# Kernel optimization log

Hardware: AMD Instinct MI355X
Metric: run time of the kernel (lower is better)

Reference implementation:

```python
import jax, jax.numpy as jnp
import numpy as np

B = 32768
F = 256
H1 = 16
H2 = 8

def setup_inputs() -> dict:
    key = jax.random.key(0)
    ks = jax.random.split(key, 9)
    x = jax.random.normal(ks[0], (B, F), dtype=jnp.float32)
    # Stacked per-feature MLP params (one UnivariateNetwork per feature)
    W1 = jax.random.normal(ks[1], (F, H1), dtype=jnp.float32) * (1.0 / np.sqrt(1))
    b1 = jax.random.normal(ks[2], (F, H1), dtype=jnp.float32) * 0.05
    W2 = jax.random.normal(ks[3], (F, H1, H2), dtype=jnp.float32) * (1.0 / np.sqrt(H1))
    b2 = jax.random.normal(ks[4], (F, H2), dtype=jnp.float32) * 0.05
    W3 = jax.random.normal(ks[5], (F, H2), dtype=jnp.float32) * (1.0 / np.sqrt(H2))
    b3 = jax.random.normal(ks[6], (F,), dtype=jnp.float32) * 0.05
    theta = jax.random.uniform(ks[7], (F,), dtype=jnp.float32) * 0.05
    bias = jnp.zeros((1,), dtype=jnp.float32)
    return {"x": x, "W1": W1, "b1": b1, "W2": W2, "b2": b2,
            "W3": W3, "b3": b3, "theta": theta, "bias": bias}

def reference(x, W1, b1, W2, b2, W3, b3, theta, bias):
    # Batched per-feature MLP: 1 -> H1 -> H2 -> 1 with ELU, all features at once.
    h1 = jax.nn.elu(x[:, :, None] * W1[None, :, :] + b1[None, :, :])      # [B, F, H1]
    h2 = jax.nn.elu(jnp.einsum('bfh,fhk->bfk', h1, W2) + b2[None, :, :])  # [B, F, H2]
    Z = jnp.einsum('bfk,fk->bf', h2, W3) + b3[None, :]                    # [B, F]
    weights = jax.nn.softplus(theta)                                      # [F]
    y_pred = Z @ weights + bias                                           # [B]
    return (y_pred, weights, Z)
```

## Files before the change

### kernel.cpp

```cpp
#include <hip/hip_runtime.h>

#define NB 32768
#define NF 256
#define H1 16
#define H2 8
#define R_PER_BLOCK 64
#define CHUNK 16

__device__ __forceinline__ float elu_f(float v) {
    return v > 0.0f ? v : (__expf(v) - 1.0f);
}

__attribute__((amdgpu_waves_per_eu(2, 2)))
__global__ __launch_bounds__(256)
void nul_kernel(const float* __restrict__ x,
                const float* __restrict__ W1, const float* __restrict__ b1,
                const float* __restrict__ W2, const float* __restrict__ b2,
                const float* __restrict__ W3, const float* __restrict__ b3,
                const float* __restrict__ theta, const float* __restrict__ bias,
                float* __restrict__ y_out, float* __restrict__ w_out,
                float* __restrict__ z_out) {
    const int f = threadIdx.x;
    const int rowBase = blockIdx.x * R_PER_BLOCK;

    float w1v[H1], b1v[H1], w2v[H1 * H2], b2v[H2], w3v[H2];
    {
        const float4* p = reinterpret_cast<const float4*>(W1 + f * H1);
        #pragma unroll
        for (int i = 0; i < H1 / 4; ++i) {
            float4 v = p[i];
            w1v[4*i] = v.x; w1v[4*i+1] = v.y; w1v[4*i+2] = v.z; w1v[4*i+3] = v.w;
        }
    }
    {
        const float4* p = reinterpret_cast<const float4*>(b1 + f * H1);
        #pragma unroll
        for (int i = 0; i < H1 / 4; ++i) {
            float4 v = p[i];
            b1v[4*i] = v.x; b1v[4*i+1] = v.y; b1v[4*i+2] = v.z; b1v[4*i+3] = v.w;
        }
    }
    {
        const float4* p = reinterpret_cast<const float4*>(W2 + f * H1 * H2);
        #pragma unroll
        for (int i = 0; i < (H1 * H2) / 4; ++i) {
            float4 v = p[i];
            w2v[4*i] = v.x; w2v[4*i+1] = v.y; w2v[4*i+2] = v.z; w2v[4*i+3] = v.w;
        }
    }
    {
        const float4* p = reinterpret_cast<const float4*>(b2 + f * H2);
        #pragma unroll
        for (int i = 0; i < H2 / 4; ++i) {
            float4 v = p[i];
            b2v[4*i] = v.x; b2v[4*i+1] = v.y; b2v[4*i+2] = v.z; b2v[4*i+3] = v.w;
        }
    }
    {
        const float4* p = reinterpret_cast<const float4*>(W3 + f * H2);
        #pragma unroll
        for (int i = 0; i < H2 / 4; ++i) {
            float4 v = p[i];
            w3v[4*i] = v.x; w3v[4*i+1] = v.y; w3v[4*i+2] = v.z; w3v[4*i+3] = v.w;
        }
    }
    const float b3v   = b3[f];
    const float th    = theta[f];
    const float wv    = __logf(1.0f + __expf(th));
    const float biasv = bias[0];

    if (blockIdx.x == 0) w_out[f] = wv;

    __shared__ float P[CHUNK][NF + 1];

    float xnext = x[rowBase * NF + f];

    for (int c = 0; c < R_PER_BLOCK; c += CHUNK) {
        #pragma unroll 1
        for (int r = 0; r < CHUNK; ++r) {
            const int row = rowBase + c + r;
            const float xv = xnext;
            int nrow = row + 1; if (nrow >= NB) nrow = row;
            xnext = x[nrow * NF + f];

            float h1v[H1];
            #pragma unroll
            for (int h = 0; h < H1; ++h)
                h1v[h] = elu_f(fmaf(xv, w1v[h], b1v[h]));

            float acc[H2];
            #pragma unroll
            for (int k = 0; k < H2; ++k) acc[k] = b2v[k];
            #pragma unroll
            for (int h = 0; h < H1; ++h) {
                #pragma unroll
                for (int k = 0; k < H2; ++k)
                    acc[k] = fmaf(h1v[h], w2v[h * H2 + k], acc[k]);
            }

            float z = b3v;
            #pragma unroll
            for (int k = 0; k < H2; ++k)
                z = fmaf(elu_f(acc[k]), w3v[k], z);

            z_out[row * NF + f] = z;
            P[r][f] = wv * z;
        }
        __syncthreads();
        {
            const int rr = threadIdx.x >> 4;
            const int l  = threadIdx.x & 15;
            float s = 0.0f;
            #pragma unroll
            for (int i = 0; i < 16; ++i) s += P[rr][i * 16 + l];
            #pragma unroll
            for (int o = 8; o > 0; o >>= 1) s += __shfl_down(s, o, 16);
            if (l == 0) y_out[rowBase + c + rr] = s + biasv;
        }
        __syncthreads();
    }
}

extern "C" void kernel_launch(void* const* d_in, const int* in_sizes, int n_in,
                              void* d_out, int out_size, void* d_ws, size_t ws_size,
                              hipStream_t stream) {
    const float* x     = (const float*)d_in[0];
    const float* W1    = (const float*)d_in[1];
    const float* b1    = (const float*)d_in[2];
    const float* W2    = (const float*)d_in[3];
    const float* b2    = (const float*)d_in[4];
    const float* W3    = (const float*)d_in[5];
    const float* b3    = (const float*)d_in[6];
    const float* theta = (const float*)d_in[7];
    const float* bias  = (const float*)d_in[8];

    float* y_out = (float*)d_out;
    float* w_out = y_out + NB;
    float* z_out = w_out + NF;

    nul_kernel<<<NB / R_PER_BLOCK, NF, 0, stream>>>(
        x, W1, b1, W2, b2, W3, b3, theta, bias, y_out, w_out, z_out);
}
```

Before: 149.6 us.

## Tile by feature groups with shared-memory weights and atomic row reduction

Replaces the one-thread-per-feature kernel, which kept all weights in registers, with a 2D grid. Each block handles 16 features and 128 rows, stages the weights in LDS, and has each thread process 8 rows in an unrolled loop to get more independent work per thread. The y reduction now uses 16-lane shuffles plus float atomics into y_out, which a separate init kernel fills with the bias first and which also computes the softplus weights. In exchange the change adds a second launch, atomic traffic, a non-deterministic summation order, and reads of x and writes of z that touch only 64 bytes per row.

```diff
diff --git a/kernel.cpp b/kernel.cpp
--- a/kernel.cpp
+++ b/kernel.cpp
@@ -4,120 +4,132 @@
 #define NF 256
 #define H1 16
 #define H2 8
-#define R_PER_BLOCK 64
-#define CHUNK 16
+#define FG 16
+#define RJ 8
+#define ROWS_PER_BLOCK (16 * RJ)
 
 __device__ __forceinline__ float elu_f(float v) {
     return v > 0.0f ? v : (__expf(v) - 1.0f);
 }
 
-__attribute__((amdgpu_waves_per_eu(2, 2)))
 __global__ __launch_bounds__(256)
-void nul_kernel(const float* __restrict__ x,
-                const float* __restrict__ W1, const float* __restrict__ b1,
-                const float* __restrict__ W2, const float* __restrict__ b2,
-                const float* __restrict__ W3, const float* __restrict__ b3,
-                const float* __restrict__ theta, const float* __restrict__ bias,
-                float* __restrict__ y_out, float* __restrict__ w_out,
-                float* __restrict__ z_out) {
-    const int f = threadIdx.x;
-    const int rowBase = blockIdx.x * R_PER_BLOCK;
+void nul_init(const float* __restrict__ theta, const float* __restrict__ bias,
+              float* __restrict__ y_out, float* __restrict__ w_out) {
+    const int t = blockIdx.x * 256 + threadIdx.x;
+    if (t < NB) y_out[t] = bias[0];
+    if (t < NF) w_out[t] = __logf(1.0f + __expf(theta[t]));
+}
 
-    float w1v[H1], b1v[H1], w2v[H1 * H2], b2v[H2], w3v[H2];
+__global__ __launch_bounds__(256)
+void nul_main(const float* __restrict__ x,
+              const float* __restrict__ W1, const float* __restrict__ b1,
+              const float* __restrict__ W2, const float* __restrict__ b2,
+              const float* __restrict__ W3, const float* __restrict__ b3,
+              const float* __restrict__ theta,
+              float* __restrict__ y_out, float* __restrict__ z_out) {
+    __shared__ __align__(16) float sW1[FG][17];
+    __shared__ __align__(16) float sB1[FG][17];
+    __shared__ __align__(16) float sW2[FG][132];
+    __shared__ __align__(16) float sB2[FG][12];
+    __shared__ __align__(16) float sW3[FG][12];
+    __shared__ float sB3[FG];
+    __shared__ float sWv[FG];
+
+    const int tid  = threadIdx.x;
+    const int f0   = blockIdx.y * FG;
+    const int row0 = blockIdx.x * ROWS_PER_BLOCK;
+
     {
-        const float4* p = reinterpret_cast<const float4*>(W1 + f * H1);
+        const int f = tid >> 4, h = tid & 15;
+        sW1[f][h] = W1[(f0 + f) * H1 + h];
+        sB1[f][h] = b1[(f0 + f) * H1 + h];
+    }
+    {
+        const int e = tid * 8;
+        const int ff = e >> 7, c = e & 127;
+        const float4* p = reinterpret_cast<const float4*>(W2 + (f0 + ff) * (H1 * H2) + c);
+        float4 v0 = p[0], v1 = p[1];
+        float* d = &sW2[ff][c];
+        d[0] = v0.x; d[1] = v0.y; d[2] = v0.z; d[3] = v0.w;
+        d[4] = v1.x; d[5] = v1.y; d[6] = v1.z; d[7] = v1.w;
+    }
+    if (tid < FG * H2) {
+        const int f = tid >> 3, k = tid & 7;
+        sB2[f][k] = b2[(f0 + f) * H2 + k];
+        sW3[f][k] = W3[(f0 + f) * H2 + k];
+    }
+    if (tid < FG) {
+        sB3[tid] = b3[f0 + tid];
+        sWv[tid] = __logf(1.0f + __expf(theta[f0 + tid]));
+    }
+    __syncthreads();
+
+    const int fl = tid & 15;
+    const int rl = tid >> 4;
+    const int f  = f0 + fl;
+
+    float xv[RJ];
+    #pragma unroll
+    for (int j = 0; j < RJ; ++j)
+        xv[j] = x[(row0 + rl + 16 * j) * NF + f];
+
+    float acc[RJ][H2];
+    {
+        const float4 ba = *reinterpret_cast<const float4*>(&sB2[fl][0]);
+        const float4 bb = *reinterpret_cast<const float4*>(&sB2[fl][4]);
         #pragma unroll
-        for (int i = 0; i < H1 / 4; ++i) {
-            float4 v = p[i];
-            w1v[4*i] = v.x; w1v[4*i+1] = v.y; w1v[4*i+2] = v.z; w1v[4*i+3] = v.w;
+        for (int j = 0; j < RJ; ++j) {
+            acc[j][0] = ba.x; acc[j][1] = ba.y; acc[j][2] = ba.z; acc[j][3] = ba.w;
+            acc[j][4] = bb.x; acc[j][5] = bb.y; acc[j][6] = bb.z; acc[j][7] = bb.w;
         }
     }
-    {
-        const float4* p = reinterpret_cast<const float4*>(b1 + f * H1);
+
+    #pragma unroll
+    for (int h = 0; h < H1; ++h) {
+        const float  w1h = sW1[fl][h];
+        const float  b1h = sB1[fl][h];
+        const float4 wa  = *reinterpret_cast<const float4*>(&sW2[fl][h * 8]);
+        const float4 wb  = *reinterpret_cast<const float4*>(&sW2[fl][h * 8 + 4]);
         #pragma unroll
-        for (int i = 0; i < H1 / 4; ++i) {
-            float4 v = p[i];
-            b1v[4*i] = v.x; b1v[4*i+1] = v.y; b1v[4*i+2] = v.z; b1v[4*i+3] = v.w;
+        for (int j = 0; j < RJ; ++j) {
+            const float h1 = elu_f(fmaf(xv[j], w1h, b1h));
+            acc[j][0] = fmaf(h1, wa.x, acc[j][0]);
+            acc[j][1] = fmaf(h1, wa.y, acc[j][1]);
+            acc[j][2] = fmaf(h1, wa.z, acc[j][2]);
+            acc[j][3] = fmaf(h1, wa.w, acc[j][3]);
+            acc[j][4] = fmaf(h1, wb.x, acc[j][4]);
+            acc[j][5] = fmaf(h1, wb.y, acc[j][5]);
+            acc[j][6] = fmaf(h1, wb.z, acc[j][6]);
+            acc[j][7] = fmaf(h1, wb.w, acc[j][7]);
         }
     }
-    {
-        const float4* p = reinterpret_cast<const float4*>(W2 + f * H1 * H2);
-        #pragma unroll
-        for (int i = 0; i < (H1 * H2) / 4; ++i) {
-            float4 v = p[i];
-            w2v[4*i] = v.x; w2v[4*i+1] = v.y; w2v[4*i+2] = v.z; w2v[4*i+3] = v.w;
-        }
-    }
-    {
-        const float4* p = reinterpret_cast<const float4*>(b2 + f * H2);
-        #pragma unroll
-        for (int i = 0; i < H2 / 4; ++i) {
-            float4 v = p[i];
-            b2v[4*i] = v.x; b2v[4*i+1] = v.y; b2v[4*i+2] = v.z; b2v[4*i+3] = v.w;
-        }
-    }
-    {
-        const float4* p = reinterpret_cast<const float4*>(W3 + f * H2);
-        #pragma unroll
-        for (int i = 0; i < H2 / 4; ++i) {
-            float4 v = p[i];
-            w3v[4*i] = v.x; w3v[4*i+1] = v.y; w3v[4*i+2] = v.z; w3v[4*i+3] = v.w;
-        }
-    }
-    const float b3v   = b3[f];
-    const float th    = theta[f];
-    const float wv    = __logf(1.0f + __expf(th));
-    const float biasv = bias[0];
 
-    if (blockIdx.x == 0) w_out[f] = wv;
+    const float4 w3a = *reinterpret_cast<const float4*>(&sW3[fl][0]);
+    const float4 w3b = *reinterpret_cast<const float4*>(&sW3[fl][4]);
+    const float  b3v = sB3[fl];
+    const float  wv  = sWv[fl];
 
-    __shared__ float P[CHUNK][NF + 1];
+    #pragma unroll
+    for (int j = 0; j < RJ; ++j) {
+        float z = b3v;
+        z = fmaf(elu_f(acc[j][0]), w3a.x, z);
+        z = fmaf(elu_f(acc[j][1]), w3a.y, z);
+        z = fmaf(elu_f(acc[j][2]), w3a.z, z);
+        z = fmaf(elu_f(acc[j][3]), w3a.w, z);
+        z = fmaf(elu_f(acc[j][4]), w3b.x, z);
+        z = fmaf(elu_f(acc[j][5]), w3b.y, z);
+        z = fmaf(elu_f(acc[j][6]), w3b.z, z);
+        z = fmaf(elu_f(acc[j][7]), w3b.w, z);
 
-    float xnext = x[rowBase * NF + f];
+        const int row = row0 + rl + 16 * j;
+        z_out[row * NF + f] = z;
 
-    for (int c = 0; c < R_PER_BLOCK; c += CHUNK) {
-        #pragma unroll 1
-        for (int r = 0; r < CHUNK; ++r) {
-            const int row = rowBase + c + r;
-            const float xv = xnext;
-            int nrow = row + 1; if (nrow >= NB) nrow = row;
-            xnext = x[nrow * NF + f];
-
-            float h1v[H1];
-            #pragma unroll
-            for (int h = 0; h < H1; ++h)
-                h1v[h] = elu_f(fmaf(xv, w1v[h], b1v[h]));
-
-            float acc[H2];
-            #pragma unroll
-            for (int k = 0; k < H2; ++k) acc[k] = b2v[k];
-            #pragma unroll
-            for (int h = 0; h < H1; ++h) {
-                #pragma unroll
-                for (int k = 0; k < H2; ++k)
-                    acc[k] = fmaf(h1v[h], w2v[h * H2 + k], acc[k]);
-            }
-
-            float z = b3v;
-            #pragma unroll
-            for (int k = 0; k < H2; ++k)
-                z = fmaf(elu_f(acc[k]), w3v[k], z);
-
-            z_out[row * NF + f] = z;
-            P[r][f] = wv * z;
-        }
-        __syncthreads();
-        {
-            const int rr = threadIdx.x >> 4;
-            const int l  = threadIdx.x & 15;
-            float s = 0.0f;
-            #pragma unroll
-            for (int i = 0; i < 16; ++i) s += P[rr][i * 16 + l];
-            #pragma unroll
-            for (int o = 8; o > 0; o >>= 1) s += __shfl_down(s, o, 16);
-            if (l == 0) y_out[rowBase + c + rr] = s + biasv;
-        }
-        __syncthreads();
+        float p = wv * z;
+        p += __shfl_xor(p, 1, 16);
+        p += __shfl_xor(p, 2, 16);
+        p += __shfl_xor(p, 4, 16);
+        p += __shfl_xor(p, 8, 16);
+        if (fl == 0) unsafeAtomicAdd(&y_out[row], p);
     }
 }
 
@@ -138,6 +150,9 @@
     float* w_out = y_out + NB;
     float* z_out = w_out + NF;
 
-    nul_kernel<<<NB / R_PER_BLOCK, NF, 0, stream>>>(
-        x, W1, b1, W2, b2, W3, b3, theta, bias, y_out, w_out, z_out);
+    nul_init<<<NB / 256, 256, 0, stream>>>(theta, bias, y_out, w_out);
+
+    dim3 grid(NB / ROWS_PER_BLOCK, NF / FG);
+    nul_main<<<grid, 256, 0, stream>>>(
+        x, W1, b1, W2, b2, W3, b3, theta, y_out, z_out);
 }
```

Measured after the change: 154.8 us. 3.5% more time.
